# Performance work log

Hardware: AMD Instinct MI355X
Metric: run time of the kernel (lower is better)

Reference implementation:

```python
import jax, jax.numpy as jnp
import numpy as np

D_MODEL = 1024
NUM_HEADS = 16
HEAD_DIM = D_MODEL // NUM_HEADS
WINDOW = 16
DILATION = 3
SCALE = HEAD_DIM ** -0.5


def _linear(x, W, b):
    # torch nn.Linear: y = x @ W.T + b, W: [out, in]
    return x @ W.T + b


def _chunk_attention(x, Wq, bq, Wk, bk, Wv, bv, chunk):
    B, L, D = x.shape
    pad = (-L) % chunk
    if pad:
        x = jnp.pad(x, ((0, 0), (0, pad), (0, 0)))
    Lp = L + pad
    nC = Lp // chunk
    xr = x.reshape(B * nC, chunk, D)  # [BC, c, D]

    def heads(t):
        return t.reshape(B * nC, chunk, NUM_HEADS, HEAD_DIM).transpose(0, 2, 1, 3)

    q = heads(_linear(xr, Wq, bq))  # [BC, H, c, hd]
    k = heads(_linear(xr, Wk, bk))
    v = heads(_linear(xr, Wv, bv))
    attn = jax.nn.softmax(jnp.einsum('bhqd,bhkd->bhqk', q, k) * SCALE, axis=-1)
    out = jnp.einsum('bhqk,bhkd->bhqd', attn, v)  # [BC, H, c, hd]
    out = out.transpose(0, 2, 1, 3).reshape(B, Lp, D)
    return out[:, :L, :]


def setup_inputs() -> dict:
    key = jax.random.key(0)
    ks = jax.random.split(key, 9)
    s = 1.0 / np.sqrt(D_MODEL)
    x = jax.random.normal(ks[0], (4, 4096, D_MODEL), dtype=jnp.float32)
    def lin(kw, kb):
        W = jax.random.uniform(kw, (D_MODEL, D_MODEL), minval=-s, maxval=s, dtype=jnp.float32)
        b = jax.random.uniform(kb, (D_MODEL,), minval=-s, maxval=s, dtype=jnp.float32)
        return W, b
    Wq, bq = lin(ks[1], ks[2])
    Wk, bk = lin(ks[3], ks[4])
    Wv, bv = lin(ks[5], ks[6])
    Wo, bo = lin(ks[7], ks[8])
    return {"x": x, "Wq": Wq, "bq": bq, "Wk": Wk, "bk": bk,
            "Wv": Wv, "bv": bv, "Wo": Wo, "bo": bo}


def reference(x, Wq, bq, Wk, bk, Wv, bv, Wo, bo):
    B, L, D = x.shape
    # local windowed attention
    local_out = _chunk_attention(x, Wq, bq, Wk, bk, Wv, bv, WINDOW)
    # dilated (atrous) attention: stride-DILATION interleave via reshape/permute
    pad = (-L) % DILATION
    x_pad = jnp.pad(x, ((0, 0), (0, pad), (0, 0))) if pad else x
    Lp = L + pad
    xv = x_pad.reshape(B, Lp // DILATION, DILATION, D).transpose(0, 2, 1, 3)
    x_atrous = xv.reshape(B * DILATION, Lp // DILATION, D)
    a = _chunk_attention(x_atrous, Wq, bq, Wk, bk, Wv, bv, WINDOW)
    a = a.reshape(B, DILATION, Lp // DILATION, D).transpose(0, 2, 1, 3).reshape(B, Lp, D)
    atrous_out = a[:, :L, :]
    return _linear(local_out + atrous_out, Wo, bo)
```

## Files before the change

### kernel.cpp

```cpp
#include <hip/hip_runtime.h>
#include <hip/hip_bf16.h>
#include <stdint.h>

typedef unsigned short ushort_t;
typedef __attribute__((ext_vector_type(8))) short bf16x8;
typedef __attribute__((ext_vector_type(4))) float f32x4;

__device__ __forceinline__ ushort_t f2bf(float f) {
    uint32_t u = __builtin_bit_cast(uint32_t, f);
    u += 0x7FFF + ((u >> 16) & 1);
    return (ushort_t)(u >> 16);
}
__device__ __forceinline__ float bf2f(ushort_t h) {
    return __builtin_bit_cast(float, (uint32_t)h << 16);
}

__device__ __forceinline__ f32x4 mfma16(bf16x8 a, bf16x8 b, f32x4 c) {
    return __builtin_amdgcn_mfma_f32_16x16x32_bf16(a, b, c, 0, 0, 0);
}

#define GLL(g, l) __builtin_amdgcn_global_load_lds(                              \
    (const __attribute__((address_space(1))) void*)(g),                          \
    (__attribute__((address_space(3))) void*)(l), 16, 0, 0)

#define CFENCE asm volatile("" ::: "memory")
#define BARRIER do { CFENCE; __builtin_amdgcn_s_barrier(); CFENCE; } while (0)
#define PRIO1 __builtin_amdgcn_s_setprio(1)
#define PRIO0 __builtin_amdgcn_s_setprio(0)
#define PH_SYNC do { BARRIER;                                                    \
    asm volatile("s_waitcnt lgkmcnt(0)" ::: "memory");                           \
    __builtin_amdgcn_sched_barrier(0); } while (0)


__device__ __forceinline__ void cvt8(const float* s, ushort_t* d) {
    float4 a = ((const float4*)s)[0], b = ((const float4*)s)[1];
    union { bf16x8 v; ushort_t u[8]; } o;
    o.u[0] = f2bf(a.x); o.u[1] = f2bf(a.y); o.u[2] = f2bf(a.z); o.u[3] = f2bf(a.w);
    o.u[4] = f2bf(b.x); o.u[5] = f2bf(b.y); o.u[6] = f2bf(b.z); o.u[7] = f2bf(b.w);
    *(bf16x8*)d = o.v;
}

__global__ __launch_bounds__(256) void cvt_all(
    const float* __restrict__ x,
    const float* __restrict__ Wq, const float* __restrict__ Wk,
    const float* __restrict__ Wv, const float* __restrict__ Wo,
    const float* __restrict__ bq, const float* __restrict__ bk,
    const float* __restrict__ bv,
    ushort_t* __restrict__ xb, ushort_t* __restrict__ wqkv,
    float* __restrict__ bqkv)
{
    const int NX = 16384 * 1024 / 8;
    const int NW = 1024 * 1024 / 8;
    int i = blockIdx.x * 256 + threadIdx.x;
    if (i < NX) {
        cvt8(x + (size_t)i * 8, xb + (size_t)i * 8);
    } else if (i < NX + 4 * NW) {
        int j = i - NX;
        int w = j >> 17, off = j & (NW - 1);
        const float* s = (w == 0) ? Wq : (w == 1) ? Wk : (w == 2) ? Wv : Wo;
        cvt8(s + (size_t)off * 8, wqkv + (size_t)j * 8);
    } else if (i < NX + 4 * NW + 384) {
        int j = i - NX - 4 * NW;
        int w2 = j >> 7, off = j & 127;
        const float* s = (w2 == 0) ? bq : (w2 == 1) ? bk : bv;
        ((float4*)(bqkv + j * 8))[0] = ((const float4*)(s + off * 8))[0];
        ((float4*)(bqkv + j * 8))[1] = ((const float4*)(s + off * 8))[1];
    }
}


#define STG(P, rb, slot, h, kt) {                                                \
    _Pragma("unroll")                                                            \
    for (int j = 0; j < 2; ++j) {                                                \
        int idx = j * 512 + tid; int row = idx >> 3, ch = idx & 7;               \
        GLL(P + (size_t)((rb) + (h) * 128 + row) * 1024 + (kt) * 64              \
              + ((ch ^ (row & 7)) * 8),                                          \
            (char*)(slot) + (size_t)idx * 16);                                   \
    } }

#define LDA4(d, mibase)                                                          \
    _Pragma("unroll")                                                            \
    for (int q = 0; q < 4; ++q)                                                  \
        _Pragma("unroll")                                                        \
        for (int kk = 0; kk < 2; ++kk)                                           \
            a[q][kk] = *(const bf16x8*)&As[(d) * 2 + wm]                         \
                [((mibase) + q) * 1024 + ln * 64 + cho[kk]];

#define LDB2(d, nibase)                                                          \
    _Pragma("unroll")                                                            \
    for (int q = 0; q < 2; ++q)                                                  \
        _Pragma("unroll")                                                        \
        for (int kk = 0; kk < 2; ++kk)                                           \
            bfr[(nibase) + q][kk] = *(const bf16x8*)&Bs[(d) * 2 + bh]            \
                [brow0 + ((nibase) + q) * 1024 + ln * 64 + cho[kk]];

#define MFMA_Q(qm, qn)                                                           \
    _Pragma("unroll")                                                            \
    for (int mi = 0; mi < 4; ++mi)                                               \
        _Pragma("unroll")                                                        \
        for (int nl = 0; nl < 2; ++nl) {                                         \
            acc[(qm)*4+mi][(qn)*2+nl] =                                          \
                mfma16(a[mi][0], bfr[(qn)*2+nl][0], acc[(qm)*4+mi][(qn)*2+nl]);  \
            acc[(qm)*4+mi][(qn)*2+nl] =                                          \
                mfma16(a[mi][1], bfr[(qn)*2+nl][1], acc[(qm)*4+mi][(qn)*2+nl]);  \
        }

template<int MODE>
__global__ __launch_bounds__(512, 2) void gemm8(
    const ushort_t* __restrict__ A, const ushort_t* __restrict__ B,
    const float* __restrict__ bias, void* __restrict__ outp,
    int M, int NTN)
{
    __shared__ ushort_t As[4][128 * 64];
    __shared__ ushort_t Bs[4][128 * 64];

    const int bid = blockIdx.x;
    const int nwg = gridDim.x;
    const int q8 = nwg >> 3;
    const int swz = (bid & 7) * q8 + (bid >> 3);
    const int m0 = (swz / NTN) * 256;
    const int n0 = (swz % NTN) * 256;

    const int tid = threadIdx.x;
    const int wave = tid >> 6, lane = tid & 63;
    const int wm = wave >> 2, wn = wave & 3;
    const int lg = lane >> 4, ln = lane & 15;
    const int bh = wn >> 1;
    const int brow0 = (wn & 1) * 4096;
    int cho[2];
    cho[0] = ((0 * 4 + lg) ^ (ln & 7)) * 8;
    cho[1] = ((1 * 4 + lg) ^ (ln & 7)) * 8;

    f32x4 acc[8][4];
#pragma unroll
    for (int i2 = 0; i2 < 8; ++i2)
#pragma unroll
        for (int j2 = 0; j2 < 4; ++j2) acc[i2][j2] = (f32x4){0.f, 0.f, 0.f, 0.f};

    STG(A, m0, &As[0][0], 0, 0)
    STG(A, m0, &As[1][0], 1, 0)
    STG(B, n0, &Bs[0][0], 0, 0)
    STG(B, n0, &Bs[1][0], 1, 0)
    STG(B, n0, &Bs[2][0], 0, 1)
    STG(B, n0, &Bs[3][0], 1, 1)
    asm volatile("s_waitcnt vmcnt(4)" ::: "memory");
    BARRIER;

    for (int i = 0; i < 8; ++i) {
        const int kA1 = 2 * i + 1;
        const int kN  = 2 * i + 2;
        const int kN1 = 2 * i + 3;
        const bool pf = (i < 7);
        bf16x8 a[4][2], bfr[4][2];

        LDA4(0, 0) LDB2(0, 0)
        STG(A, m0, &As[2][0], 0, kA1)
        PH_SYNC; PRIO1; MFMA_Q(0, 0) PRIO0;
        BARRIER;
        LDB2(0, 2)
        STG(A, m0, &As[3][0], 1, kA1)
        PH_SYNC; PRIO1; MFMA_Q(0, 1) PRIO0;
        BARRIER;
        LDA4(0, 4)
        if (pf) STG(B, n0, &Bs[0][0], 0, kN)
        PH_SYNC; PRIO1; MFMA_Q(1, 0) PRIO0;
        BARRIER;
        if (pf) STG(B, n0, &Bs[1][0], 1, kN)
        PRIO1; MFMA_Q(1, 1) PRIO0;
        if (pf) { asm volatile("s_waitcnt vmcnt(4)" ::: "memory"); }
        else    { asm volatile("s_waitcnt vmcnt(0)" ::: "memory"); }
        BARRIER;
        LDA4(1, 0) LDB2(1, 0)
        if (pf) STG(A, m0, &As[0][0], 0, kN)
        PH_SYNC; PRIO1; MFMA_Q(0, 0) PRIO0;
        BARRIER;
        LDB2(1, 2)
        if (pf) STG(A, m0, &As[1][0], 1, kN)
        PH_SYNC; PRIO1; MFMA_Q(0, 1) PRIO0;
        BARRIER;
        LDA4(1, 4)
        if (pf) STG(B, n0, &Bs[2][0], 0, kN1)
        PH_SYNC; PRIO1; MFMA_Q(1, 0) PRIO0;
        BARRIER;
        if (pf) STG(B, n0, &Bs[3][0], 1, kN1)
        PRIO1; MFMA_Q(1, 1) PRIO0;
        if (pf) { asm volatile("s_waitcnt vmcnt(4)" ::: "memory"); }
        else    { asm volatile("s_waitcnt vmcnt(0)" ::: "memory"); }
        BARRIER;
    }

#pragma unroll
    for (int ni = 0; ni < 4; ++ni) {
        int n = n0 + wn * 64 + ni * 16 + ln;
        float bval = bias[n];
#pragma unroll
        for (int mi = 0; mi < 8; ++mi) {
#pragma unroll
            for (int r = 0; r < 4; ++r) {
                int m = m0 + wm * 128 + mi * 16 + lg * 4 + r;
                float v = acc[mi][ni][r] + bval;
                if (MODE == 0) {
                    int which = n >> 10, col = n & 1023;
                    ((ushort_t*)outp)[(size_t)which * ((size_t)M * 1024)
                                      + (size_t)m * 1024 + col] = f2bf(v);
                } else {
                    ((float*)outp)[(size_t)m * 1024 + n] = v;
                }
            }
        }
    }
}


__device__ __forceinline__ bf16x8 bias8(const float* __restrict__ b, int off) {
    float4 f0 = *(const float4*)(b + off);
    float4 f1 = *(const float4*)(b + off + 4);
    union { bf16x8 v; ushort_t u[8]; } o;
    o.u[0] = f2bf(f0.x); o.u[1] = f2bf(f0.y); o.u[2] = f2bf(f0.z); o.u[3] = f2bf(f0.w);
    o.u[4] = f2bf(f1.x); o.u[5] = f2bf(f1.y); o.u[6] = f2bf(f1.z); o.u[7] = f2bf(f1.w);
    return o.v;
}


__global__ __launch_bounds__(256) void attn_local(
    const ushort_t* __restrict__ Q, const ushort_t* __restrict__ K,
    const ushort_t* __restrict__ V, ushort_t* __restrict__ S)
{
    const int wave = threadIdx.x >> 6, lane = threadIdx.x & 63;
    const int unit = blockIdx.x * 4 + wave;
    const int h = unit & 15;
    const int c = unit >> 4;
    const int g = lane >> 4, nn = lane & 15;
    __shared__ ushort_t lds_p[4][16 * 16];
    __shared__ ushort_t vt[4][64 * 16];

    const size_t rowb = (size_t)c * 16;
    size_t aoff = (rowb + nn) * 1024 + h * 64 + g * 8;
    bf16x8 qa0 = *(const bf16x8*)(Q + aoff);
    bf16x8 qa1 = *(const bf16x8*)(Q + aoff + 32);
    bf16x8 kb0 = *(const bf16x8*)(K + aoff);
    bf16x8 kb1 = *(const bf16x8*)(K + aoff + 32);
    f32x4 sc = {0.f, 0.f, 0.f, 0.f};
    sc = mfma16(qa0, kb0, sc);
    sc = mfma16(qa1, kb1, sc);

#pragma unroll
    for (int r = 0; r < 4; ++r) {
        float s = sc[r] * 0.125f;
        float mx = s;
#pragma unroll
        for (int off = 1; off < 16; off <<= 1) mx = fmaxf(mx, __shfl_xor(mx, off, 64));
        float e = __expf(s - mx);
        float sm = e;
#pragma unroll
        for (int off = 1; off < 16; off <<= 1) sm += __shfl_xor(sm, off, 64);
        lds_p[wave][(g * 4 + r) * 16 + nn] = f2bf(e / sm);
    }

#pragma unroll
    for (int it = 0; it < 2; ++it) {
        int u = it * 64 + lane;
        int n = u >> 3, cc = u & 7;
        bf16x8 vv = *(const bf16x8*)(V + (rowb + n) * 1024 + h * 64 + cc * 8);
        union { bf16x8 v; ushort_t u8[8]; } vu; vu.v = vv;
#pragma unroll
        for (int j = 0; j < 8; ++j) vt[wave][(cc * 8 + j) * 16 + n] = vu.u8[j];
    }
    __syncthreads();

    bf16x8 zero8 = {};
    bf16x8 pa = (g < 2) ? *(const bf16x8*)&lds_p[wave][nn * 16 + g * 8] : zero8;
#pragma unroll
    for (int dt = 0; dt < 4; ++dt) {
        bf16x8 vb = (g < 2) ? *(const bf16x8*)&vt[wave][(dt * 16 + nn) * 16 + g * 8] : zero8;
        f32x4 o = mfma16(pa, vb, (f32x4){0.f, 0.f, 0.f, 0.f});
#pragma unroll
        for (int r = 0; r < 4; ++r) {
            size_t orow = rowb + g * 4 + r;
            S[orow * 1024 + h * 64 + dt * 16 + nn] = f2bf(o[r]);
        }
    }
}


__global__ __launch_bounds__(256) void attn_atrous(
    const ushort_t* __restrict__ Q, const ushort_t* __restrict__ K,
    const ushort_t* __restrict__ V,
    const float* __restrict__ bq, const float* __restrict__ bk,
    const float* __restrict__ bv, ushort_t* __restrict__ S)
{
    const int wave = threadIdx.x >> 6, lane = threadIdx.x & 63;
    const int unit = blockIdx.x * 4 + wave;
    const int h = unit & 15;
    const int tmp = unit >> 4;
    const int c = tmp % 86;
    const int sidx = tmp / 86;
    const int b = sidx / 3, dil = sidx % 3;
    const int g = lane >> 4, nn = lane & 15;
    __shared__ ushort_t lds_p[4][16 * 16];
    __shared__ ushort_t vt[4][64 * 16];

    const int dof = h * 64 + g * 8;
    const int p_n = 3 * (c * 16 + nn) + dil;
    bf16x8 qa0, qa1, kb0, kb1;
    if (p_n < 4096) {
        size_t o = ((size_t)b * 4096 + p_n) * 1024 + dof;
        qa0 = *(const bf16x8*)(Q + o);
        qa1 = *(const bf16x8*)(Q + o + 32);
        kb0 = *(const bf16x8*)(K + o);
        kb1 = *(const bf16x8*)(K + o + 32);
    } else {
        qa0 = bias8(bq, dof); qa1 = bias8(bq, dof + 32);
        kb0 = bias8(bk, dof); kb1 = bias8(bk, dof + 32);
    }
    f32x4 sc = {0.f, 0.f, 0.f, 0.f};
    sc = mfma16(qa0, kb0, sc);
    sc = mfma16(qa1, kb1, sc);

#pragma unroll
    for (int r = 0; r < 4; ++r) {
        float s = sc[r] * 0.125f;
        float mx = s;
#pragma unroll
        for (int off = 1; off < 16; off <<= 1) mx = fmaxf(mx, __shfl_xor(mx, off, 64));
        float e = __expf(s - mx);
        float sm = e;
#pragma unroll
        for (int off = 1; off < 16; off <<= 1) sm += __shfl_xor(sm, off, 64);
        lds_p[wave][(g * 4 + r) * 16 + nn] = f2bf(e / sm);
    }

#pragma unroll
    for (int it = 0; it < 2; ++it) {
        int u = it * 64 + lane;
        int n = u >> 3, cc = u & 7;
        int p_v = 3 * (c * 16 + n) + dil;
        bf16x8 vv = (p_v < 4096)
            ? *(const bf16x8*)(V + ((size_t)b * 4096 + p_v) * 1024 + h * 64 + cc * 8)
            : bias8(bv, h * 64 + cc * 8);
        union { bf16x8 v; ushort_t u8[8]; } vu; vu.v = vv;
#pragma unroll
        for (int j = 0; j < 8; ++j) vt[wave][(cc * 8 + j) * 16 + n] = vu.u8[j];
    }
    __syncthreads();

    bf16x8 zero8 = {};
    bf16x8 pa = (g < 2) ? *(const bf16x8*)&lds_p[wave][nn * 16 + g * 8] : zero8;
#pragma unroll
    for (int dt = 0; dt < 4; ++dt) {
        bf16x8 vb = (g < 2) ? *(const bf16x8*)&vt[wave][(dt * 16 + nn) * 16 + g * 8] : zero8;
        f32x4 o = mfma16(pa, vb, (f32x4){0.f, 0.f, 0.f, 0.f});
#pragma unroll
        for (int r = 0; r < 4; ++r) {
            int p_q = 3 * (c * 16 + g * 4 + r) + dil;
            if (p_q < 4096) {
                size_t off = ((size_t)b * 4096 + p_q) * 1024 + h * 64 + dt * 16 + nn;
                S[off] = f2bf(bf2f(S[off]) + o[r]);
            }
        }
    }
}


extern "C" void kernel_launch(void* const* d_in, const int* in_sizes, int n_in,
                              void* d_out, int out_size, void* d_ws, size_t ws_size,
                              hipStream_t stream)
{
    const float* x  = (const float*)d_in[0];
    const float* Wq = (const float*)d_in[1];
    const float* bq = (const float*)d_in[2];
    const float* Wk = (const float*)d_in[3];
    const float* bk = (const float*)d_in[4];
    const float* Wv = (const float*)d_in[5];
    const float* bv = (const float*)d_in[6];
    const float* Wo = (const float*)d_in[7];
    const float* bo = (const float*)d_in[8];
    float* out = (float*)d_out;

    const size_t NT = 16384;
    ushort_t* xb   = (ushort_t*)d_ws;
    ushort_t* wqkv = xb + NT * 1024;
    ushort_t* wo   = wqkv + 3 * 1024 * 1024;
    ushort_t* Qb   = wo + 1024 * 1024;
    ushort_t* Kb   = Qb + NT * 1024;
    ushort_t* Vb   = Kb + NT * 1024;
    ushort_t* Sb   = Vb + NT * 1024;
    float*    bqkv = (float*)(Sb + NT * 1024);

    const int total_units = 2097152 + 4 * 131072 + 384;
    cvt_all<<<(total_units + 255) / 256, 256, 0, stream>>>(
        x, Wq, Wk, Wv, Wo, bq, bk, bv, xb, wqkv, bqkv);

    gemm8<0><<<768, 512, 0, stream>>>(xb, wqkv, bqkv, (void*)Qb, (int)NT, 12);

    attn_local <<<4096, 256, 0, stream>>>(Qb, Kb, Vb, Sb);
    attn_atrous<<<4128, 256, 0, stream>>>(Qb, Kb, Vb, bq, bk, bv, Sb);

    gemm8<1><<<256, 512, 0, stream>>>(Sb, wo, bo, (void*)out, (int)NT, 4);
}
```

Measured before the change: 378.3 us.

## Drop block barrier in attention kernels and restructure GEMM epilogue stores

```diff
diff --git a/kernel.cpp b/kernel.cpp
--- a/kernel.cpp
+++ b/kernel.cpp
@@ -28,8 +28,7 @@
 #define PRIO1 __builtin_amdgcn_s_setprio(1)
 #define PRIO0 __builtin_amdgcn_s_setprio(0)
 #define PH_SYNC do { BARRIER;                                                    \
-    asm volatile("s_waitcnt lgkmcnt(0)" ::: "memory");                           \
-    __builtin_amdgcn_sched_barrier(0); } while (0)
+    asm volatile("s_waitcnt lgkmcnt(0)" ::: "memory"); } while (0)
 
 
 __device__ __forceinline__ void cvt8(const float* s, ushort_t* d) {
@@ -189,23 +188,35 @@
         BARRIER;
     }
 
-#pragma unroll
-    for (int ni = 0; ni < 4; ++ni) {
-        int n = n0 + wn * 64 + ni * 16 + ln;
-        float bval = bias[n];
+    float bval[4];
+#pragma unroll
+    for (int ni = 0; ni < 4; ++ni) bval[ni] = bias[n0 + wn * 64 + ni * 16 + ln];
+
+    if (MODE == 0) {
+        ushort_t* obase = (ushort_t*)outp + (size_t)(n0 >> 10) * ((size_t)M * 1024)
+                          + (n0 & 1023) + wn * 64 + ln;
 #pragma unroll
         for (int mi = 0; mi < 8; ++mi) {
 #pragma unroll
             for (int r = 0; r < 4; ++r) {
                 int m = m0 + wm * 128 + mi * 16 + lg * 4 + r;
-                float v = acc[mi][ni][r] + bval;
-                if (MODE == 0) {
-                    int which = n >> 10, col = n & 1023;
-                    ((ushort_t*)outp)[(size_t)which * ((size_t)M * 1024)
-                                      + (size_t)m * 1024 + col] = f2bf(v);
-                } else {
-                    ((float*)outp)[(size_t)m * 1024 + n] = v;
-                }
+                ushort_t* orow = obase + (size_t)m * 1024;
+#pragma unroll
+                for (int ni = 0; ni < 4; ++ni)
+                    orow[ni * 16] = f2bf(acc[mi][ni][r] + bval[ni]);
+            }
+        }
+    } else {
+        float* obase = (float*)outp + n0 + wn * 64 + ln;
+#pragma unroll
+        for (int mi = 0; mi < 8; ++mi) {
+#pragma unroll
+            for (int r = 0; r < 4; ++r) {
+                int m = m0 + wm * 128 + mi * 16 + lg * 4 + r;
+                float* orow = obase + (size_t)m * 1024;
+#pragma unroll
+                for (int ni = 0; ni < 4; ++ni)
+                    orow[ni * 16] = acc[mi][ni][r] + bval[ni];
             }
         }
     }
@@ -240,22 +251,6 @@
     bf16x8 qa1 = *(const bf16x8*)(Q + aoff + 32);
     bf16x8 kb0 = *(const bf16x8*)(K + aoff);
     bf16x8 kb1 = *(const bf16x8*)(K + aoff + 32);
-    f32x4 sc = {0.f, 0.f, 0.f, 0.f};
-    sc = mfma16(qa0, kb0, sc);
-    sc = mfma16(qa1, kb1, sc);
-
-#pragma unroll
-    for (int r = 0; r < 4; ++r) {
-        float s = sc[r] * 0.125f;
-        float mx = s;
-#pragma unroll
-        for (int off = 1; off < 16; off <<= 1) mx = fmaxf(mx, __shfl_xor(mx, off, 64));
-        float e = __expf(s - mx);
-        float sm = e;
-#pragma unroll
-        for (int off = 1; off < 16; off <<= 1) sm += __shfl_xor(sm, off, 64);
-        lds_p[wave][(g * 4 + r) * 16 + nn] = f2bf(e / sm);
-    }
 
 #pragma unroll
     for (int it = 0; it < 2; ++it) {
@@ -266,7 +261,24 @@
 #pragma unroll
         for (int j = 0; j < 8; ++j) vt[wave][(cc * 8 + j) * 16 + n] = vu.u8[j];
     }
-    __syncthreads();
+
+    f32x4 sc = {0.f, 0.f, 0.f, 0.f};
+    sc = mfma16(qa0, kb0, sc);
+    sc = mfma16(qa1, kb1, sc);
+
+#pragma unroll
+    for (int r = 0; r < 4; ++r) {
+        float s = sc[r] * 0.125f;
+        float mx = s;
+#pragma unroll
+        for (int off = 1; off < 16; off <<= 1) mx = fmaxf(mx, __shfl_xor(mx, off, 64));
+        float e = __expf(s - mx);
+        float sm = e;
+#pragma unroll
+        for (int off = 1; off < 16; off <<= 1) sm += __shfl_xor(sm, off, 64);
+        lds_p[wave][(g * 4 + r) * 16 + nn] = f2bf(e / sm);
+    }
+    CFENCE;
 
     bf16x8 zero8 = {};
     bf16x8 pa = (g < 2) ? *(const bf16x8*)&lds_p[wave][nn * 16 + g * 8] : zero8;
@@ -313,22 +325,6 @@
         qa0 = bias8(bq, dof); qa1 = bias8(bq, dof + 32);
         kb0 = bias8(bk, dof); kb1 = bias8(bk, dof + 32);
     }
-    f32x4 sc = {0.f, 0.f, 0.f, 0.f};
-    sc = mfma16(qa0, kb0, sc);
-    sc = mfma16(qa1, kb1, sc);
-
-#pragma unroll
-    for (int r = 0; r < 4; ++r) {
-        float s = sc[r] * 0.125f;
-        float mx = s;
-#pragma unroll
-        for (int off = 1; off < 16; off <<= 1) mx = fmaxf(mx, __shfl_xor(mx, off, 64));
-        float e = __expf(s - mx);
-        float sm = e;
-#pragma unroll
-        for (int off = 1; off < 16; off <<= 1) sm += __shfl_xor(sm, off, 64);
-        lds_p[wave][(g * 4 + r) * 16 + nn] = f2bf(e / sm);
-    }
 
 #pragma unroll
     for (int it = 0; it < 2; ++it) {
@@ -342,7 +338,24 @@
 #pragma unroll
         for (int j = 0; j < 8; ++j) vt[wave][(cc * 8 + j) * 16 + n] = vu.u8[j];
     }
-    __syncthreads();
+
+    f32x4 sc = {0.f, 0.f, 0.f, 0.f};
+    sc = mfma16(qa0, kb0, sc);
+    sc = mfma16(qa1, kb1, sc);
+
+#pragma unroll
+    for (int r = 0; r < 4; ++r) {
+        float s = sc[r] * 0.125f;
+        float mx = s;
+#pragma unroll
+        for (int off = 1; off < 16; off <<= 1) mx = fmaxf(mx, __shfl_xor(mx, off, 64));
+        float e = __expf(s - mx);
+        float sm = e;
+#pragma unroll
+        for (int off = 1; off < 16; off <<= 1) sm += __shfl_xor(sm, off, 64);
+        lds_p[wave][(g * 4 + r) * 16 + nn] = f2bf(e / sm);
+    }
+    CFENCE;
 
     bf16x8 zero8 = {};
     bf16x8 pa = (g < 2) ? *(const bf16x8*)&lds_p[wave][nn * 16 + g * 8] : zero8;
```

After: 348.9 us. 7.8% less time.
